# Performance work log

Hardware: AMD Instinct MI355X
Metric: run time of the kernel (lower is better)

Reference implementation:

```python
import jax, jax.numpy as jnp
import numpy as np

B, X, Y, Z = 8, 128, 128, 128


def setup_inputs() -> dict:
    key = jax.random.key(0)
    k1, k2 = jax.random.split(key)
    mu = jax.random.normal(k1, (B, X, Y, Z), dtype=jnp.float32)
    active = jax.random.uniform(k2, (B, X, Y, Z), dtype=jnp.float32)
    dx = jnp.ones((1,), dtype=jnp.float32)
    return {"mu": mu, "active": active, "dx": dx}


def _lap_kernel(mu, active, dx):
    # mu, active: [X, Y, Z] single-sample grids; dx: scalar
    mu_eff = mu * active
    lap = (jnp.roll(mu_eff, 1, 0) + jnp.roll(mu_eff, -1, 0)
           + jnp.roll(mu_eff, 1, 1) + jnp.roll(mu_eff, -1, 1)
           + jnp.roll(mu_eff, 1, 2) + jnp.roll(mu_eff, -1, 2)
           - 6.0 * mu_eff) / dx ** 2
    return lap * active


def reference(mu, active, dx):
    # Faithful to Node.proces_collection: gather fields by pattern, then
    # vmap the runnable with in_axes=(0, 0, None) over the batch axis.
    out = jax.vmap(_lap_kernel, in_axes=(0, 0, None))(mu, active, dx[0])
    return out
```

## Files before the change

kernel.cpp:

```cpp
#include <hip/hip_runtime.h>

#define NB 8
#define NX 128
#define NY 128
#define NZ 128

#define TY 32
#define TX 16
#define XC (NX / TX)
#define YT (NY / TY)
#define ROWS (TY + 2)

#define EMUL(e, m, a) \
    e.x = m.x * a.x; e.y = m.y * a.y; e.z = m.z * a.z; e.w = m.w * a.w;

__global__ __launch_bounds__(1024) void lap_pipe(
    const float* __restrict__ mu,
    const float* __restrict__ act,
    const float* __restrict__ dxp,
    float* __restrict__ out)
{
    __shared__ float buf[2][ROWS][NZ];

    const int tid = threadIdx.x;
    const int bid = blockIdx.x;
    const int xc = bid & (XC - 1);
    const int yt = (bid >> 3) & (YT - 1);
    const int b  = bid >> 5;

    const int x0 = xc * TX;
    const int y0 = yt * TY;
    const int planeYZ = NY * NZ;
    const int baseB = b * NX * planeYZ;

    const float dxv = dxp[0];
    const float inv = 1.0f / (dxv * dxv);

    const int r  = tid >> 5;
    const int zq = tid & 31;
    const int z0 = zq * 4;
    const int gy = y0 + r;
    const int rowOff = gy * NZ + z0;

    const int hr   = tid >> 5;
    const int hy   = hr ? ((y0 + TY) & (NY - 1)) : ((y0 - 1) & (NY - 1));
    const int hRow = hr ? (TY + 1) : 0;
    const int hOff = hy * NZ + z0;

    float4 eP, eC, aC;
    float4 mN, aN;
    float4 mNN, aNN;
    float4 hm, ha, hmNN, haNN;

    auto ld = [&](int gx, int off, float4* m, float4* a) {
        const int gIdx = baseB + gx * planeYZ + off;
        *m = *reinterpret_cast<const float4*>(mu + gIdx);
        *a = *reinterpret_cast<const float4*>(act + gIdx);
    };

    {
        float4 m0, a0;
        ld((x0 - 1) & (NX - 1), rowOff, &m0, &a0);
        EMUL(eP, m0, a0);
        ld(x0, rowOff, &m0, &aC);
        EMUL(eC, m0, aC);
        *reinterpret_cast<float4*>(&buf[0][r + 1][z0]) = eC;
        if (tid < 64) {
            float4 m1, a1, e1;
            ld(x0, hOff, &m1, &a1);
            EMUL(e1, m1, a1);
            *reinterpret_cast<float4*>(&buf[0][hRow][z0]) = e1;
        }
        ld((x0 + 1) & (NX - 1), rowOff, &mN, &aN);
        if (tid < 64) ld((x0 + 1) & (NX - 1), hOff, &hm, &ha);
        __syncthreads();
    }

    for (int i = 0; i < TX; ++i) {
        if (i < TX - 1) {
            const int gx2 = (x0 + i + 2) & (NX - 1);
            ld(gx2, rowOff, &mNN, &aNN);
            if (tid < 64) ld(gx2, hOff, &hmNN, &haNN);
        }

        float4 eN;
        EMUL(eN, mN, aN);
        if (i < TX - 1) {
            *reinterpret_cast<float4*>(&buf[(i + 1) & 1][r + 1][z0]) = eN;
            if (tid < 64) {
                float4 he;
                EMUL(he, hm, ha);
                *reinterpret_cast<float4*>(&buf[(i + 1) & 1][hRow][z0]) = he;
            }
        }

        const int s = i & 1;
        float4 eym = *reinterpret_cast<const float4*>(&buf[s][r][z0]);
        float4 eyp = *reinterpret_cast<const float4*>(&buf[s][r + 2][z0]);
        float ezm = __shfl(eC.w, (zq + 31) & 31, 32);
        float ezp = __shfl(eC.x, (zq + 1) & 31, 32);

        float4 o;
        o.x = (eP.x + eN.x + eym.x + eyp.x + ezm  + eC.y - 6.0f * eC.x) * inv * aC.x;
        o.y = (eP.y + eN.y + eym.y + eyp.y + eC.x + eC.z - 6.0f * eC.y) * inv * aC.y;
        o.z = (eP.z + eN.z + eym.z + eyp.z + eC.y + eC.w - 6.0f * eC.z) * inv * aC.z;
        o.w = (eP.w + eN.w + eym.w + eyp.w + eC.z + ezp  - 6.0f * eC.w) * inv * aC.w;

        const int gIdx = baseB + (x0 + i) * planeYZ + rowOff;
        *reinterpret_cast<float4*>(out + gIdx) = o;

        eP = eC; eC = eN; aC = aN;
        mN = mNN; aN = aNN; hm = hmNN; ha = haNN;

        __syncthreads();
    }
}

extern "C" void kernel_launch(void* const* d_in, const int* in_sizes, int n_in,
                              void* d_out, int out_size, void* d_ws, size_t ws_size,
                              hipStream_t stream) {
    const float* mu  = (const float*)d_in[0];
    const float* act = (const float*)d_in[1];
    const float* dx  = (const float*)d_in[2];
    float* out = (float*)d_out;

    const int grid = NB * YT * XC;
    lap_pipe<<<grid, 1024, 0, stream>>>(mu, act, dx, out);
}
```

Measured before the change: 35.95 us.

## Reorder blocks and alternate x-sweep direction so neighbouring slabs share halo planes

Block index decoding is changed so that consecutive blocks cover different batch/y tiles while sharing the same x-chunk. Odd x-chunks now sweep forward and even ones backward, so adjacent chunks reach their shared boundary planes at about the same time and can reuse those halo loads from cache. Output stores become nontemporal so the write stream is less likely to evict input lines from cache. The backward sweep makes the indexing more complex, and the new schedule changes which blocks run at the same time.

```diff
diff --git a/kernel.cpp b/kernel.cpp
--- a/kernel.cpp
+++ b/kernel.cpp
@@ -11,10 +11,12 @@
 #define YT (NY / TY)
 #define ROWS (TY + 2)
 
+typedef float f4v __attribute__((ext_vector_type(4)));
+
 #define EMUL(e, m, a) \
     e.x = m.x * a.x; e.y = m.y * a.y; e.z = m.z * a.z; e.w = m.w * a.w;
 
-__global__ __launch_bounds__(1024) void lap_pipe(
+__global__ __launch_bounds__(1024) void lap_pincer(
     const float* __restrict__ mu,
     const float* __restrict__ act,
     const float* __restrict__ dxp,
@@ -24,12 +26,16 @@
 
     const int tid = threadIdx.x;
     const int bid = blockIdx.x;
-    const int xc = bid & (XC - 1);
-    const int yt = (bid >> 3) & (YT - 1);
-    const int b  = bid >> 5;
+    const int b  = bid & 7;
+    const int yt = (bid >> 3) & 3;
+    const int xc = bid >> 5;
 
     const int x0 = xc * TX;
     const int y0 = yt * TY;
+    const int fwd  = xc & 1;
+    const int start = fwd ? x0 : x0 + TX - 1;
+    const int step  = fwd ? 1 : -1;
+
     const int planeYZ = NY * NZ;
     const int baseB = b * NX * planeYZ;
 
@@ -60,25 +66,25 @@
 
     {
         float4 m0, a0;
-        ld((x0 - 1) & (NX - 1), rowOff, &m0, &a0);
+        ld((start - step) & (NX - 1), rowOff, &m0, &a0);
         EMUL(eP, m0, a0);
-        ld(x0, rowOff, &m0, &aC);
+        ld(start, rowOff, &m0, &aC);
         EMUL(eC, m0, aC);
         *reinterpret_cast<float4*>(&buf[0][r + 1][z0]) = eC;
         if (tid < 64) {
             float4 m1, a1, e1;
-            ld(x0, hOff, &m1, &a1);
+            ld(start, hOff, &m1, &a1);
             EMUL(e1, m1, a1);
             *reinterpret_cast<float4*>(&buf[0][hRow][z0]) = e1;
         }
-        ld((x0 + 1) & (NX - 1), rowOff, &mN, &aN);
-        if (tid < 64) ld((x0 + 1) & (NX - 1), hOff, &hm, &ha);
+        ld(start + step, rowOff, &mN, &aN);
+        if (tid < 64) ld(start + step, hOff, &hm, &ha);
         __syncthreads();
     }
 
     for (int i = 0; i < TX; ++i) {
         if (i < TX - 1) {
-            const int gx2 = (x0 + i + 2) & (NX - 1);
+            const int gx2 = (start + (i + 2) * step) & (NX - 1);
             ld(gx2, rowOff, &mNN, &aNN);
             if (tid < 64) ld(gx2, hOff, &hmNN, &haNN);
         }
@@ -106,8 +112,9 @@
         o.z = (eP.z + eN.z + eym.z + eyp.z + eC.y + eC.w - 6.0f * eC.z) * inv * aC.z;
         o.w = (eP.w + eN.w + eym.w + eyp.w + eC.z + ezp  - 6.0f * eC.w) * inv * aC.w;
 
-        const int gIdx = baseB + (x0 + i) * planeYZ + rowOff;
-        *reinterpret_cast<float4*>(out + gIdx) = o;
+        const int gIdx = baseB + (start + i * step) * planeYZ + rowOff;
+        f4v ov = {o.x, o.y, o.z, o.w};
+        __builtin_nontemporal_store(ov, reinterpret_cast<f4v*>(out + gIdx));
 
         eP = eC; eC = eN; aC = aN;
         mN = mNN; aN = aNN; hm = hmNN; ha = haNN;
@@ -125,5 +132,5 @@
     float* out = (float*)d_out;
 
     const int grid = NB * YT * XC;
-    lap_pipe<<<grid, 1024, 0, stream>>>(mu, act, dx, out);
+    lap_pincer<<<grid, 1024, 0, stream>>>(mu, act, dx, out);
 }
```

New measurement: 33.57 us. 6.6% less time.
